# Optimization experiments

Measured on AMD Instinct MI355X. Metric: run time of the kernel, lower is better.

## Reference

```python
import jax, jax.numpy as jnp
import numpy as np

DIM = 1024
H = 16
HD = DIM // H  # 64
BASE = 10000.0


def _rope_tables(seq_len, d):
    # freqs over half-dim, then TILED (repeat) along last axis as in the torch code
    freqs = 1.0 / (BASE ** (jnp.arange(0, d, 2, dtype=jnp.float32) / d))  # [d/2]
    t = jnp.arange(seq_len, dtype=jnp.float32)
    f = jnp.outer(t, freqs)  # [S, d/2]
    cos = jnp.concatenate([jnp.cos(f), jnp.cos(f)], axis=-1)  # [S, d] (tiled, NOT interleaved)
    sin = jnp.concatenate([jnp.sin(f), jnp.sin(f)], axis=-1)
    return cos, sin


def _apply_rope(x):
    # x: [B, H, S, d]; rotation pairs adjacent elements (2i, 2i+1)
    S, d = x.shape[-2], x.shape[-1]
    cos, sin = _rope_tables(S, d)  # [S, d]
    xh = x.reshape(*x.shape[:-1], d // 2, 2)
    x_rot = jnp.stack([-xh[..., 1], xh[..., 0]], axis=-1).reshape(x.shape)
    return x * cos + x_rot * sin


def setup_inputs() -> dict:
    key = jax.random.key(0)
    ks = jax.random.split(key, 7)
    B, Sq, Sk = 16, 512, 512
    s = 0.02
    return {
        "x": jax.random.normal(ks[0], (B, Sq, DIM), jnp.float32),
        "context": jax.random.normal(ks[1], (B, Sk, DIM), jnp.float32),
        "Wq": jax.random.normal(ks[2], (DIM, DIM), jnp.float32) * s,
        "Wk": jax.random.normal(ks[3], (DIM, DIM), jnp.float32) * s,
        "Wv": jax.random.normal(ks[4], (DIM, DIM), jnp.float32) * s,
        "Wo": jax.random.normal(ks[5], (DIM, DIM), jnp.float32) * s,
        "bo": jax.random.normal(ks[6], (DIM,), jnp.float32) * s,
    }


def reference(x, context, Wq, Wk, Wv, Wo, bo):
    B, Sq, _ = x.shape
    Sk = context.shape[1]
    scale = HD ** -0.5
    # projections, split heads: [B, H, S, HD]
    q = (x @ Wq).reshape(B, Sq, H, HD).transpose(0, 2, 1, 3)
    k = (context @ Wk).reshape(B, Sk, H, HD).transpose(0, 2, 1, 3)
    v = (context @ Wv).reshape(B, Sk, H, HD).transpose(0, 2, 1, 3)
    q = _apply_rope(q)
    k = _apply_rope(k)
    attn = jax.nn.softmax(jnp.einsum("bhqd,bhkd->bhqk", q, k) * scale, axis=-1)
    out = jnp.einsum("bhqk,bhkd->bhqd", attn, v)
    out = out.transpose(0, 2, 1, 3).reshape(B, Sq, DIM)
    return out @ Wo + bo  # dropout is identity (p=0 / eval)
```

## Files before the change

### kernel.cpp

```cpp
#include <hip/hip_runtime.h>

#define DIM   1024
#define NH    16
#define HD    64
#define BATCH 16
#define SEQ   512
#define MROWS (BATCH*SEQ)
#define SL2E  0.18033688011112042f

typedef __bf16 bf16x8 __attribute__((ext_vector_type(8)));
typedef float  floatx4 __attribute__((ext_vector_type(4)));
typedef short  short4v __attribute__((ext_vector_type(4)));

static __device__ __forceinline__ unsigned short f2bf(float f) {
    union { float f; unsigned u; } v; v.f = f;
    unsigned u = v.u;
    return (unsigned short)((u + 0x7fffu + ((u >> 16) & 1u)) >> 16);
}

static __device__ __forceinline__ void glds16(const void* g, void* l) {
    __builtin_amdgcn_global_load_lds(
        (const __attribute__((address_space(1))) unsigned int*)g,
        (__attribute__((address_space(3))) unsigned int*)l, 16, 0, 0);
}

__global__ __launch_bounds__(256)
void rope_tab(float2* __restrict__ cs)
{
    int id = blockIdx.x * blockDim.x + threadIdx.x;
    int d = id & (HD - 1), s = id >> 6;
    const float C = -0.41524101186092f;
    float f = exp2f((float)(d & 31) * C);
    float a = (float)s * f;
    cs[id] = make_float2(cosf(a), sinf(a));
}

__global__ __launch_bounds__(256)
void cvt_bf16(const float* __restrict__ X, const float* __restrict__ Cx,
              unsigned short* __restrict__ Xb, unsigned short* __restrict__ Cb)
{
    int id = blockIdx.x * blockDim.x + threadIdx.x;
    const float* src; unsigned short* dst; int e;
    if (id < (MROWS * DIM / 8)) { src = X;  dst = Xb; e = id * 8; }
    else                        { src = Cx; dst = Cb; e = (id - MROWS * DIM / 8) * 8; }
    float4 f0 = *(const float4*)&src[e];
    float4 f1 = *(const float4*)&src[e + 4];
    unsigned short o[8] = { f2bf(f0.x), f2bf(f0.y), f2bf(f0.z), f2bf(f0.w),
                            f2bf(f1.x), f2bf(f1.y), f2bf(f1.z), f2bf(f1.w) };
    *(uint4*)&dst[e] = *(const uint4*)o;
}

__global__ void transpose_w(const float* __restrict__ W0, const float* __restrict__ W1,
                            const float* __restrict__ W2, const float* __restrict__ W3,
                            unsigned short* __restrict__ T0, unsigned short* __restrict__ T1,
                            unsigned short* __restrict__ T2, unsigned short* __restrict__ T3)
{
    __shared__ float tile[32][33];
    const float* W; unsigned short* T;
    switch (blockIdx.z) {
        case 0:  W = W0; T = T0; break;
        case 1:  W = W1; T = T1; break;
        case 2:  W = W2; T = T2; break;
        default: W = W3; T = T3; break;
    }
    int n0 = blockIdx.x * 32, k0 = blockIdx.y * 32;
    int tx = threadIdx.x, ty = threadIdx.y;
    tile[ty][tx] = W[(size_t)(k0 + ty) * DIM + n0 + tx];
    __syncthreads();
    T[(size_t)(n0 + ty) * DIM + k0 + tx] = f2bf(tile[tx][ty]);
}

template <int MODE>
__global__ __launch_bounds__(256)
void gemm128(const unsigned short* __restrict__ A, const unsigned short* __restrict__ Bt,
             void* __restrict__ Out, const float* __restrict__ bias,
             const float2* __restrict__ cstab)
{
    __shared__ unsigned short As[128 * 64];
    __shared__ unsigned short Bs[128 * 64];

    const int n0 = blockIdx.x * 128;
    const int m0 = blockIdx.y * 128;
    const int t  = threadIdx.x;
    const int w = t >> 6, l = t & 63;
    const int wm = w >> 1, wn = w & 1;
    const int lane16 = l & 15, quad = l >> 4;
    const int lr = l >> 3;
    const int lc = (l & 7) * 8;

    floatx4 acc[4][4];
    #pragma unroll
    for (int mi = 0; mi < 4; mi++)
        #pragma unroll
        for (int ni = 0; ni < 4; ni++) acc[mi][ni] = (floatx4){0.f, 0.f, 0.f, 0.f};

    for (int kt = 0; kt < DIM; kt += 64) {
        #pragma unroll
        for (int j = 0; j < 4; j++) {
            int ch = w * 4 + j;
            int row = ch * 8 + lr;
            glds16(A  + (size_t)(m0 + row) * DIM + kt + lc, &As[ch * 512]);
            glds16(Bt + (size_t)(n0 + row) * DIM + kt + lc, &Bs[ch * 512]);
        }
        __syncthreads();

        #pragma unroll
        for (int kk = 0; kk < 2; kk++) {
            bf16x8 af[4], bfr[4];
            #pragma unroll
            for (int mi = 0; mi < 4; mi++)
                af[mi] = *(const bf16x8*)&As[(wm * 64 + mi * 16 + lane16) * 64 + kk * 32 + quad * 8];
            #pragma unroll
            for (int ni = 0; ni < 4; ni++)
                bfr[ni] = *(const bf16x8*)&Bs[(wn * 64 + ni * 16 + lane16) * 64 + kk * 32 + quad * 8];
            #pragma unroll
            for (int mi = 0; mi < 4; mi++)
                #pragma unroll
                for (int ni = 0; ni < 4; ni++)
                    acc[mi][ni] = __builtin_amdgcn_mfma_f32_16x16x32_bf16(af[mi], bfr[ni], acc[mi][ni], 0, 0, 0);
        }
        __syncthreads();
    }

    if (MODE == 0) {
        unsigned short* O = (unsigned short*)Out;
        #pragma unroll
        for (int ni = 0; ni < 4; ni++) {
            int n = n0 + wn * 64 + ni * 16 + lane16;
            int h = n >> 6, d = n & 63;
            #pragma unroll
            for (int mi = 0; mi < 4; mi++) {
                #pragma unroll
                for (int i = 0; i < 4; i++) {
                    int m = m0 + wm * 64 + mi * 16 + quad * 4 + i;
                    int s = m & 511, b = m >> 9;
                    float v = acc[mi][ni][i];
                    float p = __shfl_xor(v, 1, 64);
                    float2 cs = cstab[s * HD + d];
                    float r = (n & 1) ? fmaf(p, cs.y, v * cs.x) : fmaf(-p, cs.y, v * cs.x);
                    O[((size_t)(b * NH + h) * SEQ + s) * HD + d] = f2bf(r);
                }
            }
        }
    } else if (MODE == 1) {
        unsigned short* O = (unsigned short*)Out;
        #pragma unroll
        for (int mi = 0; mi < 4; mi++) {
            #pragma unroll
            for (int i = 0; i < 4; i++) {
                int m = m0 + wm * 64 + mi * 16 + quad * 4 + i;
                #pragma unroll
                for (int ni = 0; ni < 4; ni++) {
                    int n = n0 + wn * 64 + ni * 16 + lane16;
                    O[((size_t)(n >> 9) * DIM + m) * SEQ + (n & 511)] = f2bf(acc[mi][ni][i]);
                }
            }
        }
    } else {
        float* O = (float*)Out;
        #pragma unroll
        for (int ni = 0; ni < 4; ni++) {
            int n = n0 + wn * 64 + ni * 16 + lane16;
            float bv = bias[n];
            #pragma unroll
            for (int mi = 0; mi < 4; mi++) {
                #pragma unroll
                for (int i = 0; i < 4; i++) {
                    int m = m0 + wm * 64 + mi * 16 + quad * 4 + i;
                    O[(size_t)m * DIM + n] = acc[mi][ni][i] + bv;
                }
            }
        }
    }
}

__global__ __launch_bounds__(256, 4)
void attn_v3(const unsigned short* __restrict__ Q, const unsigned short* __restrict__ K,
             const unsigned short* __restrict__ Vt, unsigned short* __restrict__ Out)
{
    __shared__ unsigned short Qs[128][72];
    __shared__ unsigned short Ks[64][72];
    __shared__ unsigned short Vts[64][72];

    const int id = blockIdx.x;
    const int qi = (id >> 3) & 3;
    const int bh = (id & 7) | ((id >> 5) << 3);
    const int q0 = qi * 128;
    const int t  = threadIdx.x;
    const int w = t >> 6, l = t & 63;
    const int lane16 = l & 15, quad = l >> 4;
    const size_t base = (size_t)bh * SEQ * HD;

    const int sr = t >> 3, sc = (t & 7) * 8;
    #pragma unroll
    for (int j = 0; j < 4; j++)
        *(uint4*)&Qs[j * 32 + sr][sc] =
            *(const uint4*)&Q[base + (size_t)(q0 + j * 32 + sr) * HD + sc];

    floatx4 acc_o[2][4];
    float lsum[2] = {0.f, 0.f};
    #pragma unroll
    for (int st = 0; st < 2; st++)
        #pragma unroll
        for (int dt = 0; dt < 4; dt++) acc_o[st][dt] = (floatx4){0.f, 0.f, 0.f, 0.f};

    for (int kt = 0; kt < SEQ; kt += 64) {
        __syncthreads();
        *(uint4*)&Ks[sr][sc]       = *(const uint4*)&K[base + (size_t)(kt + sr) * HD + sc];
        *(uint4*)&Ks[sr + 32][sc]  = *(const uint4*)&K[base + (size_t)(kt + sr + 32) * HD + sc];
        *(uint4*)&Vts[sr][sc]      = *(const uint4*)&Vt[base + (size_t)sr * SEQ + kt + sc];
        *(uint4*)&Vts[sr + 32][sc] = *(const uint4*)&Vt[base + (size_t)(sr + 32) * SEQ + kt + sc];
        __syncthreads();

        short4v pa[2][4];
        #pragma unroll
        for (int st = 0; st < 2; st++) {
            floatx4 sacc[4];
            #pragma unroll
            for (int c = 0; c < 4; c++) sacc[c] = (floatx4){0.f, 0.f, 0.f, 0.f};
            #pragma unroll
            for (int kk = 0; kk < 2; kk++) {
                bf16x8 qf = *(const bf16x8*)&Qs[st * 64 + w * 16 + lane16][kk * 32 + quad * 8];
                #pragma unroll
                for (int c = 0; c < 4; c++) {
                    bf16x8 kf = *(const bf16x8*)&Ks[c * 16 + lane16][kk * 32 + quad * 8];
                    sacc[c] = __builtin_amdgcn_mfma_f32_16x16x32_bf16(kf, qf, sacc[c], 0, 0, 0);
                }
            }
            #pragma unroll
            for (int c = 0; c < 4; c++) {
                short4v pk;
                #pragma unroll
                for (int i = 0; i < 4; i++) {
                    float pv = exp2f(sacc[c][i] * SL2E);
                    lsum[st] += pv;
                    pk[i] = (short)f2bf(pv);
                }
                pa[st][c] = pk;
            }
        }
        #pragma unroll
        for (int c = 0; c < 4; c++) {
            #pragma unroll
            for (int dt = 0; dt < 4; dt++) {
                short4v vf = *(const short4v*)&Vts[dt * 16 + lane16][c * 16 + quad * 4];
                #pragma unroll
                for (int st = 0; st < 2; st++)
                    acc_o[st][dt] = __builtin_amdgcn_mfma_f32_16x16x16bf16_1k(
                        pa[st][c], vf, acc_o[st][dt], 0, 0, 0);
            }
        }
    }

    const int b = bh >> 4, h = bh & 15;
    #pragma unroll
    for (int st = 0; st < 2; st++) {
        float rs = lsum[st];
        rs += __shfl_xor(rs, 16, 64);
        rs += __shfl_xor(rs, 32, 64);
        #pragma unroll
        for (int i = 0; i < 4; i++) {
            float inv = 1.0f / __shfl(rs, quad * 4 + i, 64);
            int s = q0 + st * 64 + w * 16 + quad * 4 + i;
            #pragma unroll
            for (int dt = 0; dt < 4; dt++) {
                int d = dt * 16 + lane16;
                Out[((size_t)(b * SEQ + s)) * DIM + h * HD + d] = f2bf(acc_o[st][dt][i] * inv);
            }
        }
    }
}

extern "C" void kernel_launch(void* const* d_in, const int* in_sizes, int n_in,
                              void* d_out, int out_size, void* d_ws, size_t ws_size,
                              hipStream_t stream)
{
    const float* x   = (const float*)d_in[0];
    const float* ctx = (const float*)d_in[1];
    const float* Wq  = (const float*)d_in[2];
    const float* Wk  = (const float*)d_in[3];
    const float* Wv  = (const float*)d_in[4];
    const float* Wo  = (const float*)d_in[5];
    const float* bo  = (const float*)d_in[6];

    const size_t NW = (size_t)DIM * DIM;
    const size_t NB = (size_t)MROWS * DIM;

    unsigned short* x_bf   = (unsigned short*)d_ws;
    unsigned short* ctx_bf = x_bf + NB;
    unsigned short* WqT    = ctx_bf + NB;
    unsigned short* WkT    = WqT + NW;
    unsigned short* WvT    = WkT + NW;
    unsigned short* WoT    = WvT + NW;
    unsigned short* Kb     = WoT + NW;
    unsigned short* Vtb    = Kb + NB;
    float2*         cstab  = (float2*)(Vtb + NB);
    unsigned short* Qb     = ctx_bf;
    unsigned short* Ab     = x_bf;

    rope_tab<<<SEQ * HD / 256, 256, 0, stream>>>(cstab);
    cvt_bf16<<<2 * MROWS * DIM / 8 / 256, 256, 0, stream>>>(x, ctx, x_bf, ctx_bf);
    transpose_w<<<dim3(32, 32, 4), dim3(32, 32, 1), 0, stream>>>(
        Wq, Wk, Wv, Wo, WqT, WkT, WvT, WoT);

    gemm128<0><<<dim3(DIM / 128, MROWS / 128), 256, 0, stream>>>(ctx_bf, WkT, Kb, nullptr, cstab);
    gemm128<1><<<dim3(MROWS / 128, DIM / 128), 256, 0, stream>>>(WvT, ctx_bf, Vtb, nullptr, nullptr);
    gemm128<0><<<dim3(DIM / 128, MROWS / 128), 256, 0, stream>>>(x_bf, WqT, Qb, nullptr, cstab);

    attn_v3<<<1024, 256, 0, stream>>>(Qb, Kb, Vtb, Ab);

    gemm128<2><<<dim3(DIM / 128, MROWS / 128), 256, 0, stream>>>(Ab, WoT, d_out, bo, nullptr);
}
```

Baseline: 292.2 us.

## Fuse prep kernels, merge K/V projections, vectorize epilogues via swapped MFMA operands

Merges the three setup kernels (bf16 conversion, weight transpose, RoPE table) into one launch, and merges the K and V projections into a single grid. Swapping the MFMA operand order makes each lane hold four consecutive columns, so the RoPE, V-transpose, output and attention epilogues can do vectorized packed stores instead of scalar ones, and RoPE no longer needs a lane shuffle. The attention kernel hoists K fragment loads out of the row loop and uses incremented pointers. Rounding now uses a cheaper round-half-up bf16 conversion instead of round-to-nearest-even, which slightly changes numerics.

Result: no change. 292.0 us (-0.1%).

```diff
diff --git a/kernel.cpp b/kernel.cpp
--- a/kernel.cpp
+++ b/kernel.cpp
@@ -14,8 +14,11 @@
 
 static __device__ __forceinline__ unsigned short f2bf(float f) {
     union { float f; unsigned u; } v; v.f = f;
-    unsigned u = v.u;
-    return (unsigned short)((u + 0x7fffu + ((u >> 16) & 1u)) >> 16);
+    return (unsigned short)((v.u + 0x8000u) >> 16);
+}
+static __device__ __forceinline__ unsigned pk2(float a, float b) {
+    union { float f; unsigned u; } x, y; x.f = a; y.f = b;
+    return ((x.u + 0x8000u) >> 16) | ((y.u + 0x8000u) & 0xffff0000u);
 }
 
 static __device__ __forceinline__ void glds16(const void* g, void* l) {
@@ -25,70 +28,63 @@
 }
 
 __global__ __launch_bounds__(256)
-void rope_tab(float2* __restrict__ cs)
-{
-    int id = blockIdx.x * blockDim.x + threadIdx.x;
-    int d = id & (HD - 1), s = id >> 6;
-    const float C = -0.41524101186092f;
-    float f = exp2f((float)(d & 31) * C);
-    float a = (float)s * f;
-    cs[id] = make_float2(cosf(a), sinf(a));
-}
-
-__global__ __launch_bounds__(256)
-void cvt_bf16(const float* __restrict__ X, const float* __restrict__ Cx,
-              unsigned short* __restrict__ Xb, unsigned short* __restrict__ Cb)
-{
-    int id = blockIdx.x * blockDim.x + threadIdx.x;
-    const float* src; unsigned short* dst; int e;
-    if (id < (MROWS * DIM / 8)) { src = X;  dst = Xb; e = id * 8; }
-    else                        { src = Cx; dst = Cb; e = (id - MROWS * DIM / 8) * 8; }
-    float4 f0 = *(const float4*)&src[e];
-    float4 f1 = *(const float4*)&src[e + 4];
-    unsigned short o[8] = { f2bf(f0.x), f2bf(f0.y), f2bf(f0.z), f2bf(f0.w),
-                            f2bf(f1.x), f2bf(f1.y), f2bf(f1.z), f2bf(f1.w) };
-    *(uint4*)&dst[e] = *(const uint4*)o;
-}
-
-__global__ void transpose_w(const float* __restrict__ W0, const float* __restrict__ W1,
-                            const float* __restrict__ W2, const float* __restrict__ W3,
-                            unsigned short* __restrict__ T0, unsigned short* __restrict__ T1,
-                            unsigned short* __restrict__ T2, unsigned short* __restrict__ T3)
+void prep(const float* __restrict__ x, const float* __restrict__ ctx,
+          const float* __restrict__ Wq, const float* __restrict__ Wk,
+          const float* __restrict__ Wv, const float* __restrict__ Wo,
+          unsigned short* __restrict__ xb, unsigned short* __restrict__ cb,
+          unsigned short* __restrict__ WqT, unsigned short* __restrict__ WkT,
+          unsigned short* __restrict__ WvT, unsigned short* __restrict__ WoT,
+          float2* __restrict__ cstab)
 {
     __shared__ float tile[32][33];
-    const float* W; unsigned short* T;
-    switch (blockIdx.z) {
-        case 0:  W = W0; T = T0; break;
-        case 1:  W = W1; T = T1; break;
-        case 2:  W = W2; T = T2; break;
-        default: W = W3; T = T3; break;
-    }
-    int n0 = blockIdx.x * 32, k0 = blockIdx.y * 32;
-    int tx = threadIdx.x, ty = threadIdx.y;
-    tile[ty][tx] = W[(size_t)(k0 + ty) * DIM + n0 + tx];
-    __syncthreads();
-    T[(size_t)(n0 + ty) * DIM + k0 + tx] = f2bf(tile[tx][ty]);
-}
-
-template <int MODE>
-__global__ __launch_bounds__(256)
-void gemm128(const unsigned short* __restrict__ A, const unsigned short* __restrict__ Bt,
-             void* __restrict__ Out, const float* __restrict__ bias,
-             const float2* __restrict__ cstab)
-{
-    __shared__ unsigned short As[128 * 64];
-    __shared__ unsigned short Bs[128 * 64];
-
-    const int n0 = blockIdx.x * 128;
-    const int m0 = blockIdx.y * 128;
-    const int t  = threadIdx.x;
+    const int blk = blockIdx.x, t = threadIdx.x;
+    if (blk < 8192) {
+        const float* src = (blk < 4096) ? x : ctx;
+        unsigned short* dst = (blk < 4096) ? xb : cb;
+        int e = ((blk & 4095) * 256 + t) * 8;
+        float4 f0 = *(const float4*)&src[e];
+        float4 f1 = *(const float4*)&src[e + 4];
+        uint4 o = { pk2(f0.x, f0.y), pk2(f0.z, f0.w), pk2(f1.x, f1.y), pk2(f1.z, f1.w) };
+        *(uint4*)&dst[e] = o;
+    } else if (blk < 12288) {
+        int id2 = blk - 8192;
+        const float* W; unsigned short* T;
+        switch (id2 >> 10) {
+            case 0:  W = Wq; T = WqT; break;
+            case 1:  W = Wk; T = WkT; break;
+            case 2:  W = Wv; T = WvT; break;
+            default: W = Wo; T = WoT; break;
+        }
+        int local = id2 & 1023;
+        int n0 = (local & 31) * 32, k0 = (local >> 5) * 32;
+        int tx = t & 31, ty = t >> 5;
+        #pragma unroll
+        for (int a = 0; a < 4; a++)
+            tile[ty + 8 * a][tx] = W[(size_t)(k0 + ty + 8 * a) * DIM + n0 + tx];
+        __syncthreads();
+        #pragma unroll
+        for (int a = 0; a < 4; a++)
+            T[(size_t)(n0 + ty + 8 * a) * DIM + k0 + tx] = f2bf(tile[tx][ty + 8 * a]);
+    } else {
+        int gid = (blk - 12288) * 256 + t;
+        int d = gid & (HD - 1), s = gid >> 6;
+        const float C = -0.41524101186092f;
+        float f = exp2f((float)(d & 31) * C);
+        float a = (float)s * f;
+        cstab[gid] = make_float2(cosf(a), sinf(a));
+    }
+}
+
+static __device__ __forceinline__ void gemm_main(
+    const unsigned short* __restrict__ A, const unsigned short* __restrict__ Bt,
+    int m0, int n0, unsigned short* As, unsigned short* Bs, floatx4 acc[4][4])
+{
+    const int t = threadIdx.x;
     const int w = t >> 6, l = t & 63;
     const int wm = w >> 1, wn = w & 1;
     const int lane16 = l & 15, quad = l >> 4;
-    const int lr = l >> 3;
-    const int lc = (l & 7) * 8;
-
-    floatx4 acc[4][4];
+    const int lr = l >> 3, lc = (l & 7) * 8;
+
     #pragma unroll
     for (int mi = 0; mi < 4; mi++)
         #pragma unroll
@@ -103,7 +99,6 @@
             glds16(Bt + (size_t)(n0 + row) * DIM + kt + lc, &Bs[ch * 512]);
         }
         __syncthreads();
-
         #pragma unroll
         for (int kk = 0; kk < 2; kk++) {
             bf16x8 af[4], bfr[4];
@@ -117,65 +112,120 @@
             for (int mi = 0; mi < 4; mi++)
                 #pragma unroll
                 for (int ni = 0; ni < 4; ni++)
-                    acc[mi][ni] = __builtin_amdgcn_mfma_f32_16x16x32_bf16(af[mi], bfr[ni], acc[mi][ni], 0, 0, 0);
-        }
-        __syncthreads();
-    }
-
-    if (MODE == 0) {
-        unsigned short* O = (unsigned short*)Out;
-        #pragma unroll
-        for (int ni = 0; ni < 4; ni++) {
-            int n = n0 + wn * 64 + ni * 16 + lane16;
-            int h = n >> 6, d = n & 63;
-            #pragma unroll
-            for (int mi = 0; mi < 4; mi++) {
-                #pragma unroll
-                for (int i = 0; i < 4; i++) {
-                    int m = m0 + wm * 64 + mi * 16 + quad * 4 + i;
-                    int s = m & 511, b = m >> 9;
-                    float v = acc[mi][ni][i];
-                    float p = __shfl_xor(v, 1, 64);
-                    float2 cs = cstab[s * HD + d];
-                    float r = (n & 1) ? fmaf(p, cs.y, v * cs.x) : fmaf(-p, cs.y, v * cs.x);
-                    O[((size_t)(b * NH + h) * SEQ + s) * HD + d] = f2bf(r);
-                }
-            }
-        }
-    } else if (MODE == 1) {
-        unsigned short* O = (unsigned short*)Out;
+                    acc[mi][ni] = __builtin_amdgcn_mfma_f32_16x16x32_bf16(bfr[ni], af[mi], acc[mi][ni], 0, 0, 0);
+        }
+        __syncthreads();
+    }
+}
+
+static __device__ __forceinline__ void proj_epilogue(
+    unsigned short* __restrict__ Out, const float2* __restrict__ cstab,
+    int m0, int n0, int mode, floatx4 acc[4][4])
+{
+    const int t = threadIdx.x;
+    const int w = t >> 6, l = t & 63;
+    const int wm = w >> 1, wn = w & 1;
+    const int lane16 = l & 15, quad = l >> 4;
+
+    if (mode == 0) {
         #pragma unroll
         for (int mi = 0; mi < 4; mi++) {
-            #pragma unroll
-            for (int i = 0; i < 4; i++) {
-                int m = m0 + wm * 64 + mi * 16 + quad * 4 + i;
-                #pragma unroll
-                for (int ni = 0; ni < 4; ni++) {
-                    int n = n0 + wn * 64 + ni * 16 + lane16;
-                    O[((size_t)(n >> 9) * DIM + m) * SEQ + (n & 511)] = f2bf(acc[mi][ni][i]);
-                }
+            int m = m0 + wm * 64 + mi * 16 + lane16;
+            int s = m & 511, b = m >> 9;
+            #pragma unroll
+            for (int ni = 0; ni < 4; ni++) {
+                int n = n0 + wn * 64 + ni * 16 + quad * 4;
+                int h = n >> 6, d0 = n & 63;
+                const float4* cp = (const float4*)&cstab[s * HD + d0];
+                float4 c01 = cp[0];
+                float4 c23 = cp[1];
+                floatx4 v = acc[mi][ni];
+                float r0 = v[0] * c01.x - v[1] * c01.y;
+                float r1 = fmaf(v[0], c01.w, v[1] * c01.z);
+                float r2 = v[2] * c23.x - v[3] * c23.y;
+                float r3 = fmaf(v[2], c23.w, v[3] * c23.z);
+                uint2 o = { pk2(r0, r1), pk2(r2, r3) };
+                *(uint2*)&Out[((size_t)(b * NH + h) * SEQ + s) * HD + d0] = o;
             }
         }
     } else {
-        float* O = (float*)Out;
-        #pragma unroll
-        for (int ni = 0; ni < 4; ni++) {
-            int n = n0 + wn * 64 + ni * 16 + lane16;
-            float bv = bias[n];
-            #pragma unroll
-            for (int mi = 0; mi < 4; mi++) {
-                #pragma unroll
-                for (int i = 0; i < 4; i++) {
-                    int m = m0 + wm * 64 + mi * 16 + quad * 4 + i;
-                    O[(size_t)m * DIM + n] = acc[mi][ni][i] + bv;
-                }
-            }
+        #pragma unroll
+        for (int mi = 0; mi < 4; mi++) {
+            int m = m0 + wm * 64 + mi * 16 + lane16;
+            #pragma unroll
+            for (int ni = 0; ni < 4; ni++) {
+                int n = n0 + wn * 64 + ni * 16 + quad * 4;
+                floatx4 v = acc[mi][ni];
+                uint2 o = { pk2(v[0], v[1]), pk2(v[2], v[3]) };
+                *(uint2*)&Out[((size_t)(n >> 9) * DIM + m) * SEQ + (n & 511)] = o;
+            }
+        }
+    }
+}
+
+__global__ __launch_bounds__(256)
+void proj_kv(const unsigned short* __restrict__ cb,
+             const unsigned short* __restrict__ WkT, const unsigned short* __restrict__ WvT,
+             unsigned short* __restrict__ Kb, unsigned short* __restrict__ Vtb,
+             const float2* __restrict__ cstab)
+{
+    __shared__ unsigned short As[128 * 64];
+    __shared__ unsigned short Bs[128 * 64];
+    const unsigned short *A, *Bt; unsigned short* Out;
+    int m0, n0, mode;
+    int id = blockIdx.x;
+    if (id < 512) { A = cb;  Bt = WkT; Out = Kb;  mode = 0; n0 = (id & 7) * 128; m0 = (id >> 3) * 128; }
+    else { int i2 = id - 512;
+           A = WvT; Bt = cb;  Out = Vtb; mode = 1; m0 = (i2 & 7) * 128; n0 = (i2 >> 3) * 128; }
+    floatx4 acc[4][4];
+    gemm_main(A, Bt, m0, n0, As, Bs, acc);
+    proj_epilogue(Out, cstab, m0, n0, mode, acc);
+}
+
+__global__ __launch_bounds__(256)
+void proj_q(const unsigned short* __restrict__ xb, const unsigned short* __restrict__ WqT,
+            unsigned short* __restrict__ Qb, const float2* __restrict__ cstab)
+{
+    __shared__ unsigned short As[128 * 64];
+    __shared__ unsigned short Bs[128 * 64];
+    int id = blockIdx.x;
+    int n0 = (id & 7) * 128, m0 = (id >> 3) * 128;
+    floatx4 acc[4][4];
+    gemm_main(xb, WqT, m0, n0, As, Bs, acc);
+    proj_epilogue(Qb, cstab, m0, n0, 0, acc);
+}
+
+__global__ __launch_bounds__(256)
+void out_gemm(const unsigned short* __restrict__ Ab, const unsigned short* __restrict__ WoT,
+              float* __restrict__ O, const float* __restrict__ bias)
+{
+    __shared__ unsigned short As[128 * 64];
+    __shared__ unsigned short Bs[128 * 64];
+    int id = blockIdx.x;
+    int n0 = (id & 7) * 128, m0 = (id >> 3) * 128;
+    floatx4 acc[4][4];
+    gemm_main(Ab, WoT, m0, n0, As, Bs, acc);
+
+    const int t = threadIdx.x;
+    const int w = t >> 6, l = t & 63;
+    const int wm = w >> 1, wn = w & 1;
+    const int lane16 = l & 15, quad = l >> 4;
+    #pragma unroll
+    for (int ni = 0; ni < 4; ni++) {
+        int n = n0 + wn * 64 + ni * 16 + quad * 4;
+        float4 bv = *(const float4*)&bias[n];
+        #pragma unroll
+        for (int mi = 0; mi < 4; mi++) {
+            int m = m0 + wm * 64 + mi * 16 + lane16;
+            floatx4 v = acc[mi][ni];
+            float4 o = { v[0] + bv.x, v[1] + bv.y, v[2] + bv.z, v[3] + bv.w };
+            *(float4*)&O[(size_t)m * DIM + n] = o;
         }
     }
 }
 
 __global__ __launch_bounds__(256, 4)
-void attn_v3(const unsigned short* __restrict__ Q, const unsigned short* __restrict__ K,
+void attn_v4(const unsigned short* __restrict__ Q, const unsigned short* __restrict__ K,
              const unsigned short* __restrict__ Vt, unsigned short* __restrict__ Out)
 {
     __shared__ unsigned short Qs[128][72];
@@ -197,6 +247,11 @@
         *(uint4*)&Qs[j * 32 + sr][sc] =
             *(const uint4*)&Q[base + (size_t)(q0 + j * 32 + sr) * HD + sc];
 
+    const unsigned short* kp0 = K  + base + (size_t)sr * HD + sc;
+    const unsigned short* kp1 = kp0 + (size_t)32 * HD;
+    const unsigned short* vp0 = Vt + base + (size_t)sr * SEQ + sc;
+    const unsigned short* vp1 = vp0 + (size_t)32 * SEQ;
+
     floatx4 acc_o[2][4];
     float lsum[2] = {0.f, 0.f};
     #pragma unroll
@@ -206,11 +261,18 @@
 
     for (int kt = 0; kt < SEQ; kt += 64) {
         __syncthreads();
-        *(uint4*)&Ks[sr][sc]       = *(const uint4*)&K[base + (size_t)(kt + sr) * HD + sc];
-        *(uint4*)&Ks[sr + 32][sc]  = *(const uint4*)&K[base + (size_t)(kt + sr + 32) * HD + sc];
-        *(uint4*)&Vts[sr][sc]      = *(const uint4*)&Vt[base + (size_t)sr * SEQ + kt + sc];
-        *(uint4*)&Vts[sr + 32][sc] = *(const uint4*)&Vt[base + (size_t)(sr + 32) * SEQ + kt + sc];
-        __syncthreads();
+        *(uint4*)&Ks[sr][sc]       = *(const uint4*)kp0;  kp0 += 64 * HD;
+        *(uint4*)&Ks[sr + 32][sc]  = *(const uint4*)kp1;  kp1 += 64 * HD;
+        *(uint4*)&Vts[sr][sc]      = *(const uint4*)vp0;  vp0 += 64;
+        *(uint4*)&Vts[sr + 32][sc] = *(const uint4*)vp1;  vp1 += 64;
+        __syncthreads();
+
+        bf16x8 kf[2][4];
+        #pragma unroll
+        for (int kk = 0; kk < 2; kk++)
+            #pragma unroll
+            for (int c = 0; c < 4; c++)
+                kf[kk][c] = *(const bf16x8*)&Ks[c * 16 + lane16][kk * 32 + quad * 8];
 
         short4v pa[2][4];
         #pragma unroll
@@ -222,10 +284,8 @@
             for (int kk = 0; kk < 2; kk++) {
                 bf16x8 qf = *(const bf16x8*)&Qs[st * 64 + w * 16 + lane16][kk * 32 + quad * 8];
                 #pragma unroll
-                for (int c = 0; c < 4; c++) {
-                    bf16x8 kf = *(const bf16x8*)&Ks[c * 16 + lane16][kk * 32 + quad * 8];
-                    sacc[c] = __builtin_amdgcn_mfma_f32_16x16x32_bf16(kf, qf, sacc[c], 0, 0, 0);
-                }
+                for (int c = 0; c < 4; c++)
+                    sacc[c] = __builtin_amdgcn_mfma_f32_16x16x32_bf16(kf[kk][c], qf, sacc[c], 0, 0, 0);
             }
             #pragma unroll
             for (int c = 0; c < 4; c++) {
@@ -247,7 +307,7 @@
                 #pragma unroll
                 for (int st = 0; st < 2; st++)
                     acc_o[st][dt] = __builtin_amdgcn_mfma_f32_16x16x16bf16_1k(
-                        pa[st][c], vf, acc_o[st][dt], 0, 0, 0);
+                        vf, pa[st][c], acc_o[st][dt], 0, 0, 0);
             }
         }
     }
@@ -258,15 +318,14 @@
         float rs = lsum[st];
         rs += __shfl_xor(rs, 16, 64);
         rs += __shfl_xor(rs, 32, 64);
-        #pragma unroll
-        for (int i = 0; i < 4; i++) {
-            float inv = 1.0f / __shfl(rs, quad * 4 + i, 64);
-            int s = q0 + st * 64 + w * 16 + quad * 4 + i;
-            #pragma unroll
-            for (int dt = 0; dt < 4; dt++) {
-                int d = dt * 16 + lane16;
-                Out[((size_t)(b * SEQ + s)) * DIM + h * HD + d] = f2bf(acc_o[st][dt][i] * inv);
-            }
+        float inv = 1.0f / rs;
+        int s = q0 + st * 64 + w * 16 + lane16;
+        size_t rowbase = (size_t)(b * SEQ + s) * DIM + h * HD;
+        #pragma unroll
+        for (int dt = 0; dt < 4; dt++) {
+            floatx4 v = acc_o[st][dt];
+            uint2 o = { pk2(v[0] * inv, v[1] * inv), pk2(v[2] * inv, v[3] * inv) };
+            *(uint2*)&Out[rowbase + dt * 16 + quad * 4] = o;
         }
     }
 }
@@ -298,16 +357,13 @@
     unsigned short* Qb     = ctx_bf;
     unsigned short* Ab     = x_bf;
 
-    rope_tab<<<SEQ * HD / 256, 256, 0, stream>>>(cstab);
-    cvt_bf16<<<2 * MROWS * DIM / 8 / 256, 256, 0, stream>>>(x, ctx, x_bf, ctx_bf);
-    transpose_w<<<dim3(32, 32, 4), dim3(32, 32, 1), 0, stream>>>(
-        Wq, Wk, Wv, Wo, WqT, WkT, WvT, WoT);
-
-    gemm128<0><<<dim3(DIM / 128, MROWS / 128), 256, 0, stream>>>(ctx_bf, WkT, Kb, nullptr, cstab);
-    gemm128<1><<<dim3(MROWS / 128, DIM / 128), 256, 0, stream>>>(WvT, ctx_bf, Vtb, nullptr, nullptr);
-    gemm128<0><<<dim3(DIM / 128, MROWS / 128), 256, 0, stream>>>(x_bf, WqT, Qb, nullptr, cstab);
-
-    attn_v3<<<1024, 256, 0, stream>>>(Qb, Kb, Vtb, Ab);
-
-    gemm128<2><<<dim3(DIM / 128, MROWS / 128), 256, 0, stream>>>(Ab, WoT, d_out, bo, nullptr);
-}
+    prep<<<12416, 256, 0, stream>>>(x, ctx, Wq, Wk, Wv, Wo,
+                                    x_bf, ctx_bf, WqT, WkT, WvT, WoT, cstab);
+
+    proj_kv<<<1024, 256, 0, stream>>>(ctx_bf, WkT, WvT, Kb, Vtb, cstab);
+    proj_q<<<512, 256, 0, stream>>>(x_bf, WqT, Qb, cstab);
+
+    attn_v4<<<1024, 256, 0, stream>>>(Qb, Kb, Vtb, Ab);
+
+    out_gemm<<<512, 256, 0, stream>>>(Ab, WoT, (float*)d_out, bo);
+}
```
